# Kernel tuning notes

Measured on AMD Instinct MI355X. Metric: run time of the kernel, lower is better.

Reference implementation:

```python
import jax, jax.numpy as jnp
import numpy as np

N, C_IN, C_B, H, W, POOL = 2, 256, 128, 100, 100, 10
HW = H * W


def conv1x1(x, w, b):
    # x: [n,c,h,w], w: [o,c] -> [n,o,h,w]
    return jnp.einsum('nchw,oc->nohw', x, w) + b[None, :, None, None]


def instance_norm(x, eps=1e-5):
    # torch InstanceNorm2d(affine=False): normalize per (n,c) over spatial dims
    m = jnp.mean(x, axis=(2, 3), keepdims=True)
    v = jnp.var(x, axis=(2, 3), keepdims=True)
    return (x - m) * jax.lax.rsqrt(v + eps)


def bilinear_sample(feat, x, y, h, w):
    # feat: [n,c,h*w]; x,y: [n,p] sample coords. mmcv bilinear_interpolate semantics.
    valid = (x >= -1.0) & (x <= w) & (y >= -1.0) & (y <= h)
    x = jnp.maximum(x, 0.0)
    y = jnp.maximum(y, 0.0)
    x0f = jnp.floor(x)
    y0f = jnp.floor(y)
    cx = x0f >= w - 1
    cy = y0f >= h - 1
    x0 = jnp.where(cx, float(w - 1), x0f).astype(jnp.int32)
    y0 = jnp.where(cy, float(h - 1), y0f).astype(jnp.int32)
    x1 = jnp.minimum(x0 + 1, w - 1)
    y1 = jnp.minimum(y0 + 1, h - 1)
    xe = jnp.where(cx, x0.astype(x.dtype), x)
    ye = jnp.where(cy, y0.astype(y.dtype), y)
    lx = xe - x0
    ly = ye - y0
    hx = 1.0 - lx
    hy = 1.0 - ly

    def g(iy, ix):
        return jnp.take_along_axis(feat, (iy * w + ix)[:, None, :], axis=2)  # [n,c,p]

    val = ((hy * hx)[:, None] * g(y0, x0) + (hy * lx)[:, None] * g(y0, x1)
           + (ly * hx)[:, None] * g(y1, x0) + (ly * lx)[:, None] * g(y1, x1))
    return val * valid[:, None]


def border_align(feat, boxes, pool_size, c):
    # feat: [n,4c,h,w]; boxes: [n,hw,4]; returns [n,hw,4,c]
    n, _, h, w = feat.shape
    hw = boxes.shape[1]
    k = pool_size + 1
    t = jnp.arange(k, dtype=feat.dtype) / pool_size  # [k]
    x1, y1, x2, y2 = boxes[..., 0], boxes[..., 1], boxes[..., 2], boxes[..., 3]
    bw = x2 - x1
    bh = y2 - y1
    feat4 = feat.reshape(n, 4, c, h * w)
    # border order (mmcv): top, left, bottom, right
    xs_t = x1[..., None] + t * bw[..., None]
    ys_t = jnp.broadcast_to(y1[..., None], xs_t.shape)
    ys_l = y1[..., None] + t * bh[..., None]
    xs_l = jnp.broadcast_to(x1[..., None], ys_l.shape)
    xs_b = xs_t
    ys_b = jnp.broadcast_to(y2[..., None], xs_t.shape)
    ys_r = ys_l
    xs_r = jnp.broadcast_to(x2[..., None], ys_l.shape)
    outs = []
    for b, (xs, ys) in enumerate([(xs_t, ys_t), (xs_l, ys_l), (xs_b, ys_b), (xs_r, ys_r)]):
        v = bilinear_sample(feat4[:, b], xs.reshape(n, -1), ys.reshape(n, -1), h, w)  # [n,c,hw*k]
        outs.append(v.reshape(n, c, hw, k).max(axis=-1))  # max-pool over border points
    out = jnp.stack(outs, axis=3)  # [n,c,hw,4]
    return jnp.transpose(out, (0, 2, 3, 1))  # [n,hw,4,c]


def setup_inputs():
    key = jax.random.key(0)
    ks = jax.random.split(key, 9)
    feature = jax.random.normal(ks[0], (N, C_IN, H, W), jnp.float32)
    u = jax.random.uniform(ks[1], (N, HW, 4), jnp.float32)
    x1 = u[..., 0] * (W * 0.5)
    y1 = u[..., 1] * (H * 0.5)
    x2 = x1 + 1.0 + u[..., 2] * (W * 0.5 - 1.0)
    y2 = y1 + 1.0 + u[..., 3] * (H * 0.5 - 1.0)
    boxes = jnp.stack([x1, y1, x2, y2], axis=-1)
    wh = jax.random.uniform(ks[2], (N, HW, 2), jnp.float32) * W
    s1 = 1.0 / np.sqrt(C_IN).astype(np.float32)
    w_cur = jax.random.normal(ks[3], (C_B, C_IN), jnp.float32) * s1
    b_cur = jax.random.normal(ks[4], (C_B,), jnp.float32) * 0.01
    w_ltrb = jax.random.normal(ks[5], (4 * C_B, C_IN), jnp.float32) * s1
    b_ltrb = jax.random.normal(ks[6], (4 * C_B,), jnp.float32) * 0.01
    s2 = 1.0 / np.sqrt(5 * C_B).astype(np.float32)
    w_out = jax.random.normal(ks[7], (C_IN, 5 * C_B), jnp.float32) * s2
    b_out = jax.random.normal(ks[8], (C_IN,), jnp.float32) * 0.01
    return {"feature": feature, "boxes": boxes, "wh": wh,
            "w_cur": w_cur, "b_cur": b_cur, "w_ltrb": w_ltrb, "b_ltrb": b_ltrb,
            "w_out": w_out, "b_out": b_out}


def reference(feature, boxes, wh, w_cur, b_cur, w_ltrb, b_ltrb, w_out, b_out):
    n, _, h, w = feature.shape
    fm_short = jax.nn.relu(instance_norm(conv1x1(feature, w_cur, b_cur)))          # [n,C_B,h,w]
    ltrb = jax.nn.relu(instance_norm(conv1x1(feature, w_ltrb, b_ltrb)))            # [n,4*C_B,h,w]
    aligned = border_align(ltrb, boxes, POOL, C_B)                                  # [n,hw,4,C_B]
    # faithful to torch: permute(0,3,1,2).reshape(N,-1,H,W)
    aligned = jnp.transpose(aligned, (0, 3, 1, 2)).reshape(n, -1, h, w)             # [n,4*C_B,h,w]
    cat = jnp.concatenate([aligned, fm_short], axis=1)                              # [n,5*C_B,h,w]
    return jax.nn.relu(conv1x1(cat, w_out, b_out))                                  # [n,C_IN,h,w]
```

## Files before the change

### kernel.cpp

```cpp
#include <hip/hip_runtime.h>
#include <hip/hip_bf16.h>
#include <math.h>

#define NB    2
#define CIN   256
#define CB    128
#define HH    100
#define WW    100
#define NPIX  10000
#define CH1   640
#define K2    640
#define O2    256
#define NM    40000
#define NSAMP 11

typedef __attribute__((ext_vector_type(8))) short bf16x8;
typedef __attribute__((ext_vector_type(4))) float f32x4;
typedef unsigned short ushort_t;

__device__ __forceinline__ unsigned short f2bf(float f) {
    unsigned u = __float_as_uint(f);
    u += 0x7FFF + ((u >> 16) & 1);
    return (unsigned short)(u >> 16);
}
__device__ __forceinline__ float bf2f(ushort_t u) {
    return __uint_as_float(((unsigned)u) << 16);
}

#define MFMA16(a, b, c) __builtin_amdgcn_mfma_f32_16x16x32_bf16((a), (b), (c), 0, 0, 0)

__global__ __launch_bounds__(256) void prep_k(const float* __restrict__ wcur,
                                              const float* __restrict__ wltrb,
                                              const float* __restrict__ wout,
                                              ushort_t* __restrict__ W1b,
                                              ushort_t* __restrict__ W2b) {
    int id = blockIdx.x * 256 + threadIdx.x;
    if (id < CH1 * CIN) {
        const int ch = id / CIN;
        const float v = (ch < CB) ? wcur[id] : wltrb[id - CB * CIN];
        W1b[id] = f2bf(v);
        return;
    }
    id -= CH1 * CIN;
    if (id < O2 * K2) {
        const int o = id / K2, k = id % K2;
        const int korig = (k < 512) ? ((k & 127) * 4 + (k >> 7)) : k;
        W2b[id] = f2bf(wout[(size_t)o * K2 + korig]);
    }
}

__global__ __launch_bounds__(256) void featT_k(const float* __restrict__ feat,
                                               ushort_t* __restrict__ featTb) {
    __shared__ float T[128][65];
    const int pix0 = blockIdx.x * 64;
    const int ch0  = blockIdx.y * 128;
    const int n    = blockIdx.z;
    const int tid  = threadIdx.x;
    {
        const int pl = tid & 63, cl0 = tid >> 6;
#pragma unroll
        for (int i = 0; i < 32; ++i) {
            const int cl = cl0 + i * 4;
            const int pix = pix0 + pl;
            T[cl][pl] = (pix < NPIX)
                ? feat[((size_t)n * CIN + ch0 + cl) * NPIX + pix] : 0.f;
        }
    }
    __syncthreads();
    const int cl = tid & 127, pl0 = tid >> 7;
#pragma unroll
    for (int j = 0; j < 32; ++j) {
        const int pp = pl0 + j * 2;
        const int pix = pix0 + pp;
        if (pix < NPIX)
            featTb[((size_t)n * NPIX + pix) * CIN + ch0 + cl] = f2bf(T[cl][pp]);
    }
}

__global__ __launch_bounds__(256) void gemm1T_k(const ushort_t* __restrict__ featTb,
                                                const ushort_t* __restrict__ W1b,
                                                ushort_t* __restrict__ rawT,
                                                float* __restrict__ st) {
    __shared__ ushort_t Bs[128][40];
    const int pix0 = blockIdx.x * 128;
    const int ch0  = blockIdx.y * 128;
    const int n    = blockIdx.z;
    const int tid  = threadIdx.x;
    const int lane = tid & 63, wv = tid >> 6;
    const int wp = wv & 1, wc = wv >> 1;
    const int l15 = lane & 15, lg = lane >> 4;

    f32x4 acc[4][4];
#pragma unroll
    for (int am = 0; am < 4; ++am)
#pragma unroll
        for (int bn = 0; bn < 4; ++bn)
#pragma unroll
            for (int r = 0; r < 4; ++r) acc[am][bn][r] = 0.f;

    const int srow = tid >> 1, spart = tid & 1;
    const ushort_t* Bsrc  = featTb + (size_t)n * NPIX * CIN;
    const ushort_t* Wbase = W1b + (size_t)(ch0 + wc * 64 + l15) * CIN + lg * 8;

    uint4 pv0, pv1;
    {
        const int pix = pix0 + srow;
        pv0 = make_uint4(0, 0, 0, 0); pv1 = pv0;
        if (pix < NPIX) {
            const ushort_t* s = Bsrc + (size_t)pix * CIN + spart * 16;
            pv0 = *(const uint4*)s;
            pv1 = *(const uint4*)(s + 8);
        }
    }
#pragma unroll
    for (int ks = 0; ks < CIN / 32; ++ks) {
        const int k0 = ks * 32;
        *(uint4*)&Bs[srow][spart * 16]     = pv0;
        *(uint4*)&Bs[srow][spart * 16 + 8] = pv1;
        __syncthreads();
        if (ks + 1 < CIN / 32) {
            const int pix = pix0 + srow;
            pv0 = make_uint4(0, 0, 0, 0); pv1 = pv0;
            if (pix < NPIX) {
                const ushort_t* s = Bsrc + (size_t)pix * CIN + (k0 + 32) + spart * 16;
                pv0 = *(const uint4*)s;
                pv1 = *(const uint4*)(s + 8);
            }
        }
        bf16x8 bfrag[4];
#pragma unroll
        for (int bn = 0; bn < 4; ++bn)
            bfrag[bn] = *(const bf16x8*)(Wbase + (size_t)bn * 16 * CIN + k0);
#pragma unroll
        for (int am = 0; am < 4; ++am) {
            const bf16x8 a = *(const bf16x8*)&Bs[wp * 64 + am * 16 + l15][lg * 8];
#pragma unroll
            for (int bn = 0; bn < 4; ++bn)
                acc[am][bn] = MFMA16(a, bfrag[bn], acc[am][bn]);
        }
        __syncthreads();
    }

#pragma unroll
    for (int bn = 0; bn < 4; ++bn) {
        float s = 0.f, q = 0.f;
#pragma unroll
        for (int am = 0; am < 4; ++am)
#pragma unroll
            for (int r = 0; r < 4; ++r) { const float v = acc[am][bn][r]; s += v; q += v * v; }
        s += __shfl_xor(s, 16); q += __shfl_xor(q, 16);
        s += __shfl_xor(s, 32); q += __shfl_xor(q, 32);
        if (lg == 0) {
            const int ch = ch0 + wc * 64 + bn * 16 + l15;
            atomicAdd(&st[(size_t)(n * CH1 + ch) * 2],     s);
            atomicAdd(&st[(size_t)(n * CH1 + ch) * 2 + 1], q);
        }
    }

#pragma unroll
    for (int am = 0; am < 4; ++am)
#pragma unroll
        for (int r = 0; r < 4; ++r) {
            const int pix = pix0 + wp * 64 + am * 16 + lg * 4 + r;
            if (pix < NPIX) {
                ushort_t* dst = rawT + (size_t)(n * NPIX + pix) * CH1 + ch0 + wc * 64 + l15;
#pragma unroll
                for (int bn = 0; bn < 4; ++bn) dst[bn * 16] = f2bf(acc[am][bn][r]);
            }
        }
}

__global__ __launch_bounds__(256) void stfin_k(const float* __restrict__ st,
                                               float2* __restrict__ MS) {
    const int ch = blockIdx.x * 256 + threadIdx.x;
    if (ch >= NB * CH1) return;
    const float sum = st[(size_t)ch * 2];
    const float sq  = st[(size_t)ch * 2 + 1];
    const float m   = sum * (1.0f / (float)NPIX);
    const float var = fmaxf(sq * (1.0f / (float)NPIX) - m * m, 0.f);
    MS[ch] = make_float2(m, 1.0f / sqrtf(var + 1e-5f));
}

__global__ __launch_bounds__(256) void norm4_k(const ushort_t* __restrict__ rawT,
                                               const float2* __restrict__ MS,
                                               ushort_t* __restrict__ CATb) {
    const int id = blockIdx.x * 256 + threadIdx.x;
    if (id >= NB * NPIX * 16) return;
    const int c8 = (id & 15) * 8;
    const int np = id >> 4;
    const int n = np / NPIX, pix = np % NPIX;
    const uint4 v = *(const uint4*)(rawT + (size_t)np * CH1 + c8);
    ushort_t tmp[8]; *(uint4*)tmp = v;
    ushort_t outv[8];
    const float2* msb = MS + n * CH1 + c8;
#pragma unroll
    for (int j = 0; j < 8; ++j) {
        const float2 ms = msb[j];
        const float x = (bf2f(tmp[j]) - ms.x) * ms.y;
        outv[j] = f2bf(fmaxf(x, 0.f));
    }
    *(uint4*)(CATb + ((size_t)(n * 5 + 4) * NPIX + pix) * 128 + c8) = *(uint4*)outv;
}

__global__ __launch_bounds__(256) void coord_k(const float* __restrict__ boxes,
                                               int* __restrict__ OFFS,
                                               float4* __restrict__ WTS) {
    const int id = blockIdx.x * 256 + threadIdx.x;
    if (id >= NB * NM * NSAMP) return;
    const int k  = id % NSAMP;
    const int mm = id / NSAMP;
    const int m  = mm % NM;
    const int n  = mm / NM;
    const int p = m >> 2, b = m & 3;
    const float* bx = boxes + ((size_t)n * NPIX + p) * 4;
    const float x1 = bx[0], y1 = bx[1], x2 = bx[2], y2 = bx[3];
    const float bw = __fsub_rn(x2, x1), bh = __fsub_rn(y2, y1);
    const float t = __fdiv_rn((float)k, 10.0f);
    float x, y;
    if (b == 0)      { x = __fadd_rn(x1, __fmul_rn(t, bw)); y = y1; }
    else if (b == 1) { x = x1; y = __fadd_rn(y1, __fmul_rn(t, bh)); }
    else if (b == 2) { x = __fadd_rn(x1, __fmul_rn(t, bw)); y = y2; }
    else             { x = x2; y = __fadd_rn(y1, __fmul_rn(t, bh)); }
    const bool valid = (x >= -1.f) && (x <= (float)WW) && (y >= -1.f) && (y <= (float)HH);
    x = fmaxf(x, 0.f); y = fmaxf(y, 0.f);
    const float x0f = floorf(x), y0f = floorf(y);
    const bool cx = (x0f >= (float)(WW - 1));
    const bool cy = (y0f >= (float)(HH - 1));
    const int ix0 = cx ? (WW - 1) : (int)x0f;
    const int iy0 = cy ? (HH - 1) : (int)y0f;
    const int ix1 = min(ix0 + 1, WW - 1);
    const int iy1 = min(iy0 + 1, HH - 1);
    const float lx = cx ? 0.f : __fsub_rn(x, (float)ix0);
    const float ly = cy ? 0.f : __fsub_rn(y, (float)iy0);
    const float hx = 1.f - lx, hy = 1.f - ly;
    const float vf = valid ? 1.f : 0.f;
    const int dx = ix1 - ix0, dy = iy1 - iy0;
    const int did = (((n * 4 + b) * NPIX) + p) * NSAMP + k;
    OFFS[did] = (iy0 * WW + ix0) | (dx << 14) | (dy << 15);
    WTS[did]  = make_float4((hy * hx) * vf, (hy * lx) * vf,
                            (ly * hx) * vf, (ly * lx) * vf);
}

__global__ __launch_bounds__(256) void borderN_k(const int* __restrict__ OFFS,
                                                 const float4* __restrict__ WTS,
                                                 const ushort_t* __restrict__ rawT,
                                                 const float2* __restrict__ MS,
                                                 ushort_t* __restrict__ CATb) {
    const int s = blockIdx.x & 7;
    const int n = s >> 2, b = s & 3;
    const int u = threadIdx.x >> 5;
    const int c4 = (threadIdx.x & 31) * 4;
    const int p = (blockIdx.x >> 3) * 8 + u;
    const int chb = CB + b * CB + c4;
    const float4 q0 = *(const float4*)(MS + n * CH1 + chb);
    const float4 q1 = *(const float4*)(MS + n * CH1 + chb + 2);
    const ushort_t* base = rawT + (size_t)n * NPIX * CH1 + chb;
    const int dbase = (((n * 4 + b) * NPIX) + p) * NSAMP;
    float ax = -INFINITY, ay = -INFINITY, az = -INFINITY, aw = -INFINITY;
#pragma unroll
    for (int k = 0; k < NSAMP; ++k) {
        const int    v  = OFFS[dbase + k];
        const float4 wt = WTS[dbase + k];
        const int off = v & 0x3FFF;
        const int dxo = ((v >> 14) & 1) * CH1;
        const int dyo = ((v >> 15) & 1) * (WW * CH1);
        const ushort_t* t00 = base + (size_t)off * CH1;
        const ushort4 u00 = *(const ushort4*)(t00);
        const ushort4 u01 = *(const ushort4*)(t00 + dxo);
        const ushort4 u10 = *(const ushort4*)(t00 + dyo);
        const ushort4 u11 = *(const ushort4*)(t00 + dyo + dxo);
        float s0 = wt.x * fmaxf(bf2f(u00.x) - q0.x, 0.f);
        float s1 = wt.x * fmaxf(bf2f(u00.y) - q0.z, 0.f);
        float s2 = wt.x * fmaxf(bf2f(u00.z) - q1.x, 0.f);
        float s3 = wt.x * fmaxf(bf2f(u00.w) - q1.z, 0.f);
        s0 = fmaf(wt.y, fmaxf(bf2f(u01.x) - q0.x, 0.f), s0);
        s1 = fmaf(wt.y, fmaxf(bf2f(u01.y) - q0.z, 0.f), s1);
        s2 = fmaf(wt.y, fmaxf(bf2f(u01.z) - q1.x, 0.f), s2);
        s3 = fmaf(wt.y, fmaxf(bf2f(u01.w) - q1.z, 0.f), s3);
        s0 = fmaf(wt.z, fmaxf(bf2f(u10.x) - q0.x, 0.f), s0);
        s1 = fmaf(wt.z, fmaxf(bf2f(u10.y) - q0.z, 0.f), s1);
        s2 = fmaf(wt.z, fmaxf(bf2f(u10.z) - q1.x, 0.f), s2);
        s3 = fmaf(wt.z, fmaxf(bf2f(u10.w) - q1.z, 0.f), s3);
        s0 = fmaf(wt.w, fmaxf(bf2f(u11.x) - q0.x, 0.f), s0);
        s1 = fmaf(wt.w, fmaxf(bf2f(u11.y) - q0.z, 0.f), s1);
        s2 = fmaf(wt.w, fmaxf(bf2f(u11.z) - q1.x, 0.f), s2);
        s3 = fmaf(wt.w, fmaxf(bf2f(u11.w) - q1.z, 0.f), s3);
        ax = fmaxf(ax, q0.y * s0); ay = fmaxf(ay, q0.w * s1);
        az = fmaxf(az, q1.y * s2); aw = fmaxf(aw, q1.w * s3);
    }
    const int m = p * 4 + b;
    ushort_t* dst = CATb + ((size_t)n * 5 * NPIX + m) * 128 + c4;
    dst[0] = f2bf(ax); dst[1] = f2bf(ay); dst[2] = f2bf(az); dst[3] = f2bf(aw);
}

__global__ __launch_bounds__(256) void gemm2_k(const ushort_t* __restrict__ W2b,
                                               const ushort_t* __restrict__ CATb,
                                               const float* __restrict__ bout,
                                               float* __restrict__ out) {
    __shared__ ushort_t Bs[128][40];
    const int pix0 = blockIdx.x * 128;
    const int o0   = blockIdx.y * 64;
    const int n    = blockIdx.z;
    const int tid  = threadIdx.x;
    const int lane = tid & 63, wv = tid >> 6;
    const int wo = wv & 1, wp = wv >> 1;
    const int l15 = lane & 15, lg = lane >> 4;

    f32x4 acc[2][4];
#pragma unroll
    for (int am = 0; am < 2; ++am)
#pragma unroll
        for (int bn = 0; bn < 4; ++bn)
#pragma unroll
            for (int r = 0; r < 4; ++r) acc[am][bn][r] = 0.f;

    const int srow = tid >> 1, spart = tid & 1;
    const ushort_t* CATn = CATb + (size_t)n * 5 * NPIX * 128;
    const ushort_t* A0 = W2b + (size_t)(o0 + wo * 32 + l15) * K2 + lg * 8;
    const ushort_t* A1 = A0 + 16 * K2;

    uint4 pv0, pv1;
    {
        const int pix = pix0 + srow;
        pv0 = make_uint4(0, 0, 0, 0); pv1 = pv0;
        if (pix < NPIX) {
            const ushort_t* s = CATn + (size_t)pix * 128 + spart * 16;
            pv0 = *(const uint4*)s;
            pv1 = *(const uint4*)(s + 8);
        }
    }
#pragma unroll
    for (int ks = 0; ks < K2 / 32; ++ks) {
        const int k0 = ks * 32;
        *(uint4*)&Bs[srow][spart * 16]     = pv0;
        *(uint4*)&Bs[srow][spart * 16 + 8] = pv1;
        __syncthreads();
        if (ks + 1 < K2 / 32) {
            const int k0n = k0 + 32;
            const int slot = k0n >> 7, c0 = k0n & 127;
            const int pix = pix0 + srow;
            pv0 = make_uint4(0, 0, 0, 0); pv1 = pv0;
            if (pix < NPIX) {
                const ushort_t* s = CATn + ((size_t)slot * NPIX + pix) * 128 + c0 + spart * 16;
                pv0 = *(const uint4*)s;
                pv1 = *(const uint4*)(s + 8);
            }
        }
        const bf16x8 a0 = *(const bf16x8*)(A0 + k0);
        const bf16x8 a1 = *(const bf16x8*)(A1 + k0);
#pragma unroll
        for (int bn = 0; bn < 4; ++bn) {
            const bf16x8 b = *(const bf16x8*)&Bs[wp * 64 + bn * 16 + l15][lg * 8];
            acc[0][bn] = MFMA16(a0, b, acc[0][bn]);
            acc[1][bn] = MFMA16(a1, b, acc[1][bn]);
        }
        __syncthreads();
    }

    const int obase = o0 + wo * 32 + lg * 4;
#pragma unroll
    for (int am = 0; am < 2; ++am) {
        const float4 bi = *(const float4*)&bout[obase + am * 16];
#pragma unroll
        for (int bn = 0; bn < 4; ++bn) {
            const int pix = pix0 + wp * 64 + bn * 16 + l15;
            if (pix < NPIX) {
                float* dst = out + ((size_t)n * O2 + obase + am * 16) * NPIX + pix;
                dst[0 * (size_t)NPIX] = fmaxf(acc[am][bn][0] + bi.x, 0.f);
                dst[1 * (size_t)NPIX] = fmaxf(acc[am][bn][1] + bi.y, 0.f);
                dst[2 * (size_t)NPIX] = fmaxf(acc[am][bn][2] + bi.z, 0.f);
                dst[3 * (size_t)NPIX] = fmaxf(acc[am][bn][3] + bi.w, 0.f);
            }
        }
    }
}

extern "C" void kernel_launch(void* const* d_in, const int* in_sizes, int n_in,
                              void* d_out, int out_size, void* d_ws, size_t ws_size,
                              hipStream_t stream) {
    const float* feature = (const float*)d_in[0];
    const float* boxes   = (const float*)d_in[1];
    const float* w_cur   = (const float*)d_in[3];
    const float* w_ltrb  = (const float*)d_in[5];
    const float* w_out   = (const float*)d_in[7];
    const float* b_out   = (const float*)d_in[8];
    float* out = (float*)d_out;

    float* ws = (float*)d_ws;
    float*    st     = ws;
    float2*   MS     = (float2*)(st + NB * CH1 * 2);
    ushort_t* featTb = (ushort_t*)(MS + NB * CH1);
    ushort_t* rawT   = featTb + (size_t)NB * NPIX * CIN;
    ushort_t* CATb   = rawT + (size_t)NB * NPIX * CH1;
    ushort_t* W1b    = CATb + (size_t)NB * 5 * NPIX * 128;
    ushort_t* W2b    = W1b + CH1 * CIN;
    int*      OFFS   = (int*)(W2b + O2 * K2);
    float4*   WTS    = (float4*)(OFFS + NB * NM * NSAMP);

    hipMemsetAsync(st, 0, (size_t)NB * CH1 * 2 * sizeof(float), stream);
    prep_k<<<(CH1 * CIN + O2 * K2 + 255) / 256, 256, 0, stream>>>(w_cur, w_ltrb, w_out, W1b, W2b);
    featT_k<<<dim3((NPIX + 63) / 64, 2, NB), 256, 0, stream>>>(feature, featTb);
    gemm1T_k<<<dim3((NPIX + 127) / 128, CH1 / 128, NB), 256, 0, stream>>>(featTb, W1b, rawT, st);
    stfin_k<<<(NB * CH1 + 255) / 256, 256, 0, stream>>>(st, MS);
    norm4_k<<<(NB * NPIX * 16 + 255) / 256, 256, 0, stream>>>(rawT, MS, CATb);
    coord_k<<<(NB * NM * NSAMP + 255) / 256, 256, 0, stream>>>(boxes, OFFS, WTS);
    borderN_k<<<NB * 4 * NPIX / 8, 256, 0, stream>>>(OFFS, WTS, rawT, MS, CATb);
    gemm2_k<<<dim3((NPIX + 127) / 128, O2 / 64, NB), 256, 0, stream>>>(W2b, CATb, b_out, out);
}
```

Measured before the change: 247.2 us.

## Pre-normalize ltrb into per-border planar buffer and deepen GEMM K-stages

The normalize kernel now applies instance norm and ReLU to all 640 channels, writing the 512 ltrb channels into a separate per-border, channel-contiguous bf16 buffer. The border-align kernel can then gather 16-byte vectors of already-normalized values instead of strided 8-byte loads with per-tap normalization math. Both GEMMs also stage 64 K-values per barrier using two LDS halves, which halves the number of synchronizations. The cost is an extra full write and read of the normalized ltrb tensor, more LDS per block, and higher register pressure.

```diff
diff --git a/kernel.cpp b/kernel.cpp
--- a/kernel.cpp
+++ b/kernel.cpp
@@ -81,7 +81,7 @@
                                                 const ushort_t* __restrict__ W1b,
                                                 ushort_t* __restrict__ rawT,
                                                 float* __restrict__ st) {
-    __shared__ ushort_t Bs[128][40];
+    __shared__ ushort_t Bs[2][128][40];
     const int pix0 = blockIdx.x * 128;
     const int ch0  = blockIdx.y * 128;
     const int n    = blockIdx.z;
@@ -99,44 +99,48 @@
             for (int r = 0; r < 4; ++r) acc[am][bn][r] = 0.f;
 
     const int srow = tid >> 1, spart = tid & 1;
+    const int spix = pix0 + srow;
     const ushort_t* Bsrc  = featTb + (size_t)n * NPIX * CIN;
     const ushort_t* Wbase = W1b + (size_t)(ch0 + wc * 64 + l15) * CIN + lg * 8;
 
-    uint4 pv0, pv1;
+    uint4 pv0, pv1, pv2, pv3;
     {
-        const int pix = pix0 + srow;
-        pv0 = make_uint4(0, 0, 0, 0); pv1 = pv0;
-        if (pix < NPIX) {
-            const ushort_t* s = Bsrc + (size_t)pix * CIN + spart * 16;
-            pv0 = *(const uint4*)s;
-            pv1 = *(const uint4*)(s + 8);
-        }
-    }
-#pragma unroll
-    for (int ks = 0; ks < CIN / 32; ++ks) {
-        const int k0 = ks * 32;
-        *(uint4*)&Bs[srow][spart * 16]     = pv0;
-        *(uint4*)&Bs[srow][spart * 16 + 8] = pv1;
+        pv0 = make_uint4(0, 0, 0, 0); pv1 = pv0; pv2 = pv0; pv3 = pv0;
+        if (spix < NPIX) {
+            const ushort_t* s = Bsrc + (size_t)spix * CIN + spart * 16;
+            pv0 = *(const uint4*)s;       pv1 = *(const uint4*)(s + 8);
+            pv2 = *(const uint4*)(s + 32); pv3 = *(const uint4*)(s + 40);
+        }
+    }
+#pragma unroll
+    for (int ks = 0; ks < CIN / 64; ++ks) {
+        *(uint4*)&Bs[0][srow][spart * 16]     = pv0;
+        *(uint4*)&Bs[0][srow][spart * 16 + 8] = pv1;
+        *(uint4*)&Bs[1][srow][spart * 16]     = pv2;
+        *(uint4*)&Bs[1][srow][spart * 16 + 8] = pv3;
         __syncthreads();
-        if (ks + 1 < CIN / 32) {
-            const int pix = pix0 + srow;
-            pv0 = make_uint4(0, 0, 0, 0); pv1 = pv0;
-            if (pix < NPIX) {
-                const ushort_t* s = Bsrc + (size_t)pix * CIN + (k0 + 32) + spart * 16;
-                pv0 = *(const uint4*)s;
-                pv1 = *(const uint4*)(s + 8);
-            }
-        }
-        bf16x8 bfrag[4];
-#pragma unroll
-        for (int bn = 0; bn < 4; ++bn)
-            bfrag[bn] = *(const bf16x8*)(Wbase + (size_t)bn * 16 * CIN + k0);
-#pragma unroll
-        for (int am = 0; am < 4; ++am) {
-            const bf16x8 a = *(const bf16x8*)&Bs[wp * 64 + am * 16 + l15][lg * 8];
+        if (ks + 1 < CIN / 64) {
+            pv0 = make_uint4(0, 0, 0, 0); pv1 = pv0; pv2 = pv0; pv3 = pv0;
+            if (spix < NPIX) {
+                const ushort_t* s = Bsrc + (size_t)spix * CIN + (ks + 1) * 64 + spart * 16;
+                pv0 = *(const uint4*)s;       pv1 = *(const uint4*)(s + 8);
+                pv2 = *(const uint4*)(s + 32); pv3 = *(const uint4*)(s + 40);
+            }
+        }
+#pragma unroll
+        for (int half = 0; half < 2; ++half) {
+            const int k0 = ks * 64 + half * 32;
+            bf16x8 bfrag[4];
 #pragma unroll
             for (int bn = 0; bn < 4; ++bn)
-                acc[am][bn] = MFMA16(a, bfrag[bn], acc[am][bn]);
+                bfrag[bn] = *(const bf16x8*)(Wbase + (size_t)bn * 16 * CIN + k0);
+#pragma unroll
+            for (int am = 0; am < 4; ++am) {
+                const bf16x8 a = *(const bf16x8*)&Bs[half][wp * 64 + am * 16 + l15][lg * 8];
+#pragma unroll
+                for (int bn = 0; bn < 4; ++bn)
+                    acc[am][bn] = MFMA16(a, bfrag[bn], acc[am][bn]);
+            }
         }
         __syncthreads();
     }
@@ -181,13 +185,14 @@
     MS[ch] = make_float2(m, 1.0f / sqrtf(var + 1e-5f));
 }
 
-__global__ __launch_bounds__(256) void norm4_k(const ushort_t* __restrict__ rawT,
-                                               const float2* __restrict__ MS,
-                                               ushort_t* __restrict__ CATb) {
+__global__ __launch_bounds__(256) void normAll_k(const ushort_t* __restrict__ rawT,
+                                                 const float2* __restrict__ MS,
+                                                 ushort_t* __restrict__ CATb,
+                                                 ushort_t* __restrict__ Lb) {
     const int id = blockIdx.x * 256 + threadIdx.x;
-    if (id >= NB * NPIX * 16) return;
-    const int c8 = (id & 15) * 8;
-    const int np = id >> 4;
+    if (id >= NB * NPIX * 80) return;
+    const int c8 = (id % 80) * 8;
+    const int np = id / 80;
     const int n = np / NPIX, pix = np % NPIX;
     const uint4 v = *(const uint4*)(rawT + (size_t)np * CH1 + c8);
     ushort_t tmp[8]; *(uint4*)tmp = v;
@@ -199,7 +204,15 @@
         const float x = (bf2f(tmp[j]) - ms.x) * ms.y;
         outv[j] = f2bf(fmaxf(x, 0.f));
     }
-    *(uint4*)(CATb + ((size_t)(n * 5 + 4) * NPIX + pix) * 128 + c8) = *(uint4*)outv;
+    ushort_t* dst;
+    if (c8 < 128) {
+        dst = CATb + ((size_t)(n * 5 + 4) * NPIX + pix) * 128 + c8;
+    } else {
+        const int b  = (c8 - 128) >> 7;
+        const int cc = (c8 - 128) & 127;
+        dst = Lb + ((size_t)((n * 4 + b) * NPIX) + pix) * 128 + cc;
+    }
+    *(uint4*)dst = *(uint4*)outv;
 }
 
 __global__ __launch_bounds__(256) void coord_k(const float* __restrict__ boxes,
@@ -241,63 +254,56 @@
                             (ly * hx) * vf, (ly * lx) * vf);
 }
 
-__global__ __launch_bounds__(256) void borderN_k(const int* __restrict__ OFFS,
+__global__ __launch_bounds__(256) void borderB_k(const int* __restrict__ OFFS,
                                                  const float4* __restrict__ WTS,
-                                                 const ushort_t* __restrict__ rawT,
-                                                 const float2* __restrict__ MS,
+                                                 const ushort_t* __restrict__ Lb,
                                                  ushort_t* __restrict__ CATb) {
     const int s = blockIdx.x & 7;
     const int n = s >> 2, b = s & 3;
-    const int u = threadIdx.x >> 5;
-    const int c4 = (threadIdx.x & 31) * 4;
-    const int p = (blockIdx.x >> 3) * 8 + u;
-    const int chb = CB + b * CB + c4;
-    const float4 q0 = *(const float4*)(MS + n * CH1 + chb);
-    const float4 q1 = *(const float4*)(MS + n * CH1 + chb + 2);
-    const ushort_t* base = rawT + (size_t)n * NPIX * CH1 + chb;
+    const int u = threadIdx.x >> 4;
+    const int c8 = (threadIdx.x & 15) * 8;
+    const int p = (blockIdx.x >> 3) * 16 + u;
+    const ushort_t* Lbase = Lb + ((size_t)(n * 4 + b) * NPIX) * 128 + c8;
     const int dbase = (((n * 4 + b) * NPIX) + p) * NSAMP;
-    float ax = -INFINITY, ay = -INFINITY, az = -INFINITY, aw = -INFINITY;
+    float a0 = -INFINITY, a1 = -INFINITY, a2 = -INFINITY, a3 = -INFINITY;
+    float a4 = -INFINITY, a5 = -INFINITY, a6 = -INFINITY, a7 = -INFINITY;
 #pragma unroll
     for (int k = 0; k < NSAMP; ++k) {
         const int    v  = OFFS[dbase + k];
         const float4 wt = WTS[dbase + k];
         const int off = v & 0x3FFF;
-        const int dxo = ((v >> 14) & 1) * CH1;
-        const int dyo = ((v >> 15) & 1) * (WW * CH1);
-        const ushort_t* t00 = base + (size_t)off * CH1;
-        const ushort4 u00 = *(const ushort4*)(t00);
-        const ushort4 u01 = *(const ushort4*)(t00 + dxo);
-        const ushort4 u10 = *(const ushort4*)(t00 + dyo);
-        const ushort4 u11 = *(const ushort4*)(t00 + dyo + dxo);
-        float s0 = wt.x * fmaxf(bf2f(u00.x) - q0.x, 0.f);
-        float s1 = wt.x * fmaxf(bf2f(u00.y) - q0.z, 0.f);
-        float s2 = wt.x * fmaxf(bf2f(u00.z) - q1.x, 0.f);
-        float s3 = wt.x * fmaxf(bf2f(u00.w) - q1.z, 0.f);
-        s0 = fmaf(wt.y, fmaxf(bf2f(u01.x) - q0.x, 0.f), s0);
-        s1 = fmaf(wt.y, fmaxf(bf2f(u01.y) - q0.z, 0.f), s1);
-        s2 = fmaf(wt.y, fmaxf(bf2f(u01.z) - q1.x, 0.f), s2);
-        s3 = fmaf(wt.y, fmaxf(bf2f(u01.w) - q1.z, 0.f), s3);
-        s0 = fmaf(wt.z, fmaxf(bf2f(u10.x) - q0.x, 0.f), s0);
-        s1 = fmaf(wt.z, fmaxf(bf2f(u10.y) - q0.z, 0.f), s1);
-        s2 = fmaf(wt.z, fmaxf(bf2f(u10.z) - q1.x, 0.f), s2);
-        s3 = fmaf(wt.z, fmaxf(bf2f(u10.w) - q1.z, 0.f), s3);
-        s0 = fmaf(wt.w, fmaxf(bf2f(u11.x) - q0.x, 0.f), s0);
-        s1 = fmaf(wt.w, fmaxf(bf2f(u11.y) - q0.z, 0.f), s1);
-        s2 = fmaf(wt.w, fmaxf(bf2f(u11.z) - q1.x, 0.f), s2);
-        s3 = fmaf(wt.w, fmaxf(bf2f(u11.w) - q1.z, 0.f), s3);
-        ax = fmaxf(ax, q0.y * s0); ay = fmaxf(ay, q0.w * s1);
-        az = fmaxf(az, q1.y * s2); aw = fmaxf(aw, q1.w * s3);
+        const int dxo = ((v >> 14) & 1) * 128;
+        const int dyo = ((v >> 15) & 1) * (WW * 128);
+        const ushort_t* t = Lbase + (size_t)off * 128;
+        ushort_t g00[8], g01[8], g10[8], g11[8];
+        *(uint4*)g00 = *(const uint4*)(t);
+        *(uint4*)g01 = *(const uint4*)(t + dxo);
+        *(uint4*)g10 = *(const uint4*)(t + dyo);
+        *(uint4*)g11 = *(const uint4*)(t + dyo + dxo);
+#define TAPJ(j, accv)                                                        \
+        {                                                                    \
+            float val = wt.x * bf2f(g00[j]);                                 \
+            val = fmaf(wt.y, bf2f(g01[j]), val);                             \
+            val = fmaf(wt.z, bf2f(g10[j]), val);                             \
+            val = fmaf(wt.w, bf2f(g11[j]), val);                             \
+            accv = fmaxf(accv, val);                                         \
+        }
+        TAPJ(0, a0) TAPJ(1, a1) TAPJ(2, a2) TAPJ(3, a3)
+        TAPJ(4, a4) TAPJ(5, a5) TAPJ(6, a6) TAPJ(7, a7)
+#undef TAPJ
     }
     const int m = p * 4 + b;
-    ushort_t* dst = CATb + ((size_t)n * 5 * NPIX + m) * 128 + c4;
-    dst[0] = f2bf(ax); dst[1] = f2bf(ay); dst[2] = f2bf(az); dst[3] = f2bf(aw);
+    ushort_t outv[8];
+    outv[0] = f2bf(a0); outv[1] = f2bf(a1); outv[2] = f2bf(a2); outv[3] = f2bf(a3);
+    outv[4] = f2bf(a4); outv[5] = f2bf(a5); outv[6] = f2bf(a6); outv[7] = f2bf(a7);
+    *(uint4*)(CATb + ((size_t)n * 5 * NPIX + m) * 128 + c8) = *(uint4*)outv;
 }
 
 __global__ __launch_bounds__(256) void gemm2_k(const ushort_t* __restrict__ W2b,
                                                const ushort_t* __restrict__ CATb,
                                                const float* __restrict__ bout,
                                                float* __restrict__ out) {
-    __shared__ ushort_t Bs[128][40];
+    __shared__ ushort_t Bs[2][128][40];
     const int pix0 = blockIdx.x * 128;
     const int o0   = blockIdx.y * 64;
     const int n    = blockIdx.z;
@@ -315,47 +321,54 @@
             for (int r = 0; r < 4; ++r) acc[am][bn][r] = 0.f;
 
     const int srow = tid >> 1, spart = tid & 1;
+    const int spix = pix0 + srow;
     const ushort_t* CATn = CATb + (size_t)n * 5 * NPIX * 128;
     const ushort_t* A0 = W2b + (size_t)(o0 + wo * 32 + l15) * K2 + lg * 8;
     const ushort_t* A1 = A0 + 16 * K2;
 
-    uint4 pv0, pv1;
+#define G2ADDR(j) (CATn + ((size_t)((j) >> 2) * NPIX + spix) * 128 + (((j) & 3) * 32) + spart * 16)
+
+    uint4 pv0, pv1, pv2, pv3;
     {
-        const int pix = pix0 + srow;
-        pv0 = make_uint4(0, 0, 0, 0); pv1 = pv0;
-        if (pix < NPIX) {
-            const ushort_t* s = CATn + (size_t)pix * 128 + spart * 16;
-            pv0 = *(const uint4*)s;
-            pv1 = *(const uint4*)(s + 8);
-        }
-    }
-#pragma unroll
-    for (int ks = 0; ks < K2 / 32; ++ks) {
-        const int k0 = ks * 32;
-        *(uint4*)&Bs[srow][spart * 16]     = pv0;
-        *(uint4*)&Bs[srow][spart * 16 + 8] = pv1;
+        pv0 = make_uint4(0, 0, 0, 0); pv1 = pv0; pv2 = pv0; pv3 = pv0;
+        if (spix < NPIX) {
+            const ushort_t* s0 = G2ADDR(0);
+            const ushort_t* s1 = G2ADDR(1);
+            pv0 = *(const uint4*)s0; pv1 = *(const uint4*)(s0 + 8);
+            pv2 = *(const uint4*)s1; pv3 = *(const uint4*)(s1 + 8);
+        }
+    }
+#pragma unroll
+    for (int ks = 0; ks < K2 / 64; ++ks) {
+        *(uint4*)&Bs[0][srow][spart * 16]     = pv0;
+        *(uint4*)&Bs[0][srow][spart * 16 + 8] = pv1;
+        *(uint4*)&Bs[1][srow][spart * 16]     = pv2;
+        *(uint4*)&Bs[1][srow][spart * 16 + 8] = pv3;
         __syncthreads();
-        if (ks + 1 < K2 / 32) {
-            const int k0n = k0 + 32;
-            const int slot = k0n >> 7, c0 = k0n & 127;
-            const int pix = pix0 + srow;
-            pv0 = make_uint4(0, 0, 0, 0); pv1 = pv0;
-            if (pix < NPIX) {
-                const ushort_t* s = CATn + ((size_t)slot * NPIX + pix) * 128 + c0 + spart * 16;
-                pv0 = *(const uint4*)s;
-                pv1 = *(const uint4*)(s + 8);
-            }
-        }
-        const bf16x8 a0 = *(const bf16x8*)(A0 + k0);
-        const bf16x8 a1 = *(const bf16x8*)(A1 + k0);
-#pragma unroll
-        for (int bn = 0; bn < 4; ++bn) {
-            const bf16x8 b = *(const bf16x8*)&Bs[wp * 64 + bn * 16 + l15][lg * 8];
-            acc[0][bn] = MFMA16(a0, b, acc[0][bn]);
-            acc[1][bn] = MFMA16(a1, b, acc[1][bn]);
+        if (ks + 1 < K2 / 64) {
+            pv0 = make_uint4(0, 0, 0, 0); pv1 = pv0; pv2 = pv0; pv3 = pv0;
+            if (spix < NPIX) {
+                const ushort_t* s0 = G2ADDR(2 * ks + 2);
+                const ushort_t* s1 = G2ADDR(2 * ks + 3);
+                pv0 = *(const uint4*)s0; pv1 = *(const uint4*)(s0 + 8);
+                pv2 = *(const uint4*)s1; pv3 = *(const uint4*)(s1 + 8);
+            }
+        }
+#pragma unroll
+        for (int half = 0; half < 2; ++half) {
+            const int k0 = ks * 64 + half * 32;
+            const bf16x8 af0 = *(const bf16x8*)(A0 + k0);
+            const bf16x8 af1 = *(const bf16x8*)(A1 + k0);
+#pragma unroll
+            for (int bn = 0; bn < 4; ++bn) {
+                const bf16x8 bfr = *(const bf16x8*)&Bs[half][wp * 64 + bn * 16 + l15][lg * 8];
+                acc[0][bn] = MFMA16(af0, bfr, acc[0][bn]);
+                acc[1][bn] = MFMA16(af1, bfr, acc[1][bn]);
+            }
         }
         __syncthreads();
     }
+#undef G2ADDR
 
     const int obase = o0 + wo * 32 + lg * 4;
 #pragma unroll
@@ -392,7 +405,8 @@
     ushort_t* featTb = (ushort_t*)(MS + NB * CH1);
     ushort_t* rawT   = featTb + (size_t)NB * NPIX * CIN;
     ushort_t* CATb   = rawT + (size_t)NB * NPIX * CH1;
-    ushort_t* W1b    = CATb + (size_t)NB * 5 * NPIX * 128;
+    ushort_t* Lb     = CATb + (size_t)NB * 5 * NPIX * 128;
+    ushort_t* W1b    = Lb + (size_t)NB * 4 * NPIX * 128;
     ushort_t* W2b    = W1b + CH1 * CIN;
     int*      OFFS   = (int*)(W2b + O2 * K2);
     float4*   WTS    = (float4*)(OFFS + NB * NM * NSAMP);
@@ -402,8 +416,8 @@
     featT_k<<<dim3((NPIX + 63) / 64, 2, NB), 256, 0, stream>>>(feature, featTb);
     gemm1T_k<<<dim3((NPIX + 127) / 128, CH1 / 128, NB), 256, 0, stream>>>(featTb, W1b, rawT, st);
     stfin_k<<<(NB * CH1 + 255) / 256, 256, 0, stream>>>(st, MS);
-    norm4_k<<<(NB * NPIX * 16 + 255) / 256, 256, 0, stream>>>(rawT, MS, CATb);
+    normAll_k<<<(NB * NPIX * 80 + 255) / 256, 256, 0, stream>>>(rawT, MS, CATb, Lb);
     coord_k<<<(NB * NM * NSAMP + 255) / 256, 256, 0, stream>>>(boxes, OFFS, WTS);
-    borderN_k<<<NB * 4 * NPIX / 8, 256, 0, stream>>>(OFFS, WTS, rawT, MS, CATb);
+    borderB_k<<<NB * 4 * NPIX / 16, 256, 0, stream>>>(OFFS, WTS, Lb, CATb);
     gemm2_k<<<dim3((NPIX + 127) / 128, O2 / 64, NB), 256, 0, stream>>>(W2b, CATb, b_out, out);
 }
```

After: 221.8 us. -10.3%, faster.
